# Performance work log

Hardware: AMD Instinct MI355X
Metric: run time of the kernel (lower is better)

## Reference

```python
import jax, jax.numpy as jnp
import numpy as np

BATCH, T, HID = 4, 2048, 1024
H = P = 1024  # input_dim and ssm_size (expand_ratio=1.0)
EPS = 1e-5
DISCRETIZATION = "IM"  # 'IM' or 'IMEX'


def setup_inputs() -> dict:
    key = jax.random.key(0)
    ks = jax.random.split(key, 10)
    std_b = 1.0 / np.sqrt(H)
    std_c = 1.0 / np.sqrt(P)
    u = lambda k, s, lo, hi: jax.random.uniform(k, s, jnp.float32, lo, hi)
    return {
        "hidden_states": jax.random.normal(ks[0], (BATCH, T, HID), jnp.float32),
        "Wi": jax.random.normal(ks[1], (H, HID), jnp.float32) / np.sqrt(HID),
        "Wg": jax.random.normal(ks[2], (H, HID), jnp.float32) / np.sqrt(HID),
        "Wo": jax.random.normal(ks[3], (HID, H), jnp.float32) / np.sqrt(H),
        "A_diag": u(ks[4], (P,), 0.0, 1.0),
        "B_param": u(ks[5], (P, H, 2), -std_b, std_b),
        "C_param": u(ks[6], (H, P, 2), -std_c, std_c),
        "D": jax.random.normal(ks[7], (H,), jnp.float32),
        "dt": u(ks[8], (P,), 0.0, 1.0),
        "norm_weight": jnp.ones((H,), jnp.float32),
    }


def _linoss(x, B_param, C_param, A_diag, dt_p, D):
    """LinOSS oscillatory SSM recurrence with complex B/C and diagonal A.
    x: (B,T,H) real input. State z,y in C^P (re/im stacked on last axis)."""
    A = jax.nn.relu(A_diag)       # (P,) nonneg frequencies
    dt = jax.nn.sigmoid(dt_p)     # (P,) timesteps in (0,1)
    # Bu_{re,im}[b,t,p] = sum_h x[b,t,h] * B_{re,im}[p,h]
    Bu = jnp.einsum('bth,phc->btpc', x, B_param)  # (B,T,P,2)
    if DISCRETIZATION == "IM":
        S = 1.0 / (1.0 + dt * dt * A)
        m11, m12, m21, m22 = S, -dt * A * S, dt * S, S
        f1, f2 = dt * S, dt * dt * S
    else:  # IMEX
        one = jnp.ones_like(dt)
        m11, m12, m21, m22 = one, -dt * A, dt, 1.0 - dt * dt * A
        f1, f2 = dt, dt * dt
    c = lambda v: v[None, :, None]  # broadcast (P,) -> (B,P,2)

    def step(carry, bu):
        z, y = carry  # each (B,P,2)
        z1 = c(m11) * z + c(m12) * y + c(f1) * bu
        y1 = c(m21) * z + c(m22) * y + c(f2) * bu
        return (z1, y1), y1

    z0 = jnp.zeros((x.shape[0], A.shape[0], 2), x.dtype)
    _, ys = jax.lax.scan(step, (z0, z0), jnp.swapaxes(Bu, 0, 1))
    ys = jnp.swapaxes(ys, 0, 1)  # (B,T,P,2)
    # o = Re(C @ y) + D * x
    o = (jnp.einsum('btp,hp->bth', ys[..., 0], C_param[..., 0])
         - jnp.einsum('btp,hp->bth', ys[..., 1], C_param[..., 1]))
    return o + x * D


def reference(hidden_states, Wi, Wg, Wo, A_diag, B_param, C_param, D, dt, norm_weight):
    x = hidden_states @ Wi.T                        # i_proj
    o = _linoss(x, B_param, C_param, A_diag, dt, D)  # fused_recurrent_linoss
    g = hidden_states @ Wg.T                        # g_proj
    # FusedRMSNormGated: rmsnorm(o) * weight * swish(g)
    o = o * jax.lax.rsqrt(jnp.mean(o * o, axis=-1, keepdims=True) + EPS) * norm_weight
    o = o * (g * jax.nn.sigmoid(g))
    return o @ Wo.T                                  # o_proj
```

## Files before the change

kernel.cpp:

```cpp
#include <hip/hip_runtime.h>
#include <hip/hip_bf16.h>
#include <math.h>

#define BB 4
#define TT 2048
#define HH 1024
#define PP 1024
#define MT 8192
#define C2 2048
#define NC 64
#define LCH 32

typedef __attribute__((ext_vector_type(8))) short  bf16x8;
typedef __attribute__((ext_vector_type(4))) float  f32x4;

__device__ __forceinline__ ushort f2bf(float f) {
    union { float f; unsigned u; } v; v.f = f;
    unsigned r = v.u + 0x7fffu + ((v.u >> 16) & 1u);
    return (ushort)(r >> 16);
}
__device__ __forceinline__ float bf2f(ushort h) {
    union { unsigned u; float f; } v; v.u = ((unsigned)h) << 16;
    return v.f;
}

__device__ __forceinline__ void gload16(const ushort* g, ushort* l) {
    __builtin_amdgcn_global_load_lds((const __attribute__((address_space(1))) void*)g,
                                     (__attribute__((address_space(3))) void*)l,
                                     16, 0, 0);
}
__device__ __forceinline__ void barrier_raw() { __builtin_amdgcn_s_barrier(); }
__device__ __forceinline__ void lgk0() { asm volatile("s_waitcnt lgkmcnt(0)" ::: "memory"); }
__device__ __forceinline__ void vm4()  { asm volatile("s_waitcnt vmcnt(4)"   ::: "memory"); }
__device__ __forceinline__ void vm6()  { asm volatile("s_waitcnt vmcnt(6)"   ::: "memory"); }
__device__ __forceinline__ void vm0()  { asm volatile("s_waitcnt vmcnt(0)"   ::: "memory"); }

__global__ void convert_all(const float* __restrict__ hs, const float* __restrict__ Wi,
                            const float* __restrict__ Wg, const float* __restrict__ Wo,
                            ushort* __restrict__ hsb, ushort* __restrict__ Wigb,
                            ushort* __restrict__ Wob) {
    int i = blockIdx.x * 256 + threadIdx.x;
    const int HS4 = MT * HH / 4;
    const int W4  = HH * HH / 4;
    const float4* s;
    ushort4* d;
    if (i < HS4)               { s = (const float4*)hs + i;               d = (ushort4*)hsb  + i; }
    else if (i < HS4 + 2 * W4) { int j = i - HS4;
                                 s = (const float4*)(j < W4 ? Wi : Wg) + (j < W4 ? j : j - W4);
                                 d = (ushort4*)Wigb + j; }
    else                       { int j = i - HS4 - 2 * W4;
                                 s = (const float4*)Wo + j;               d = (ushort4*)Wob + j; }
    float4 v = *s;
    ushort4 o;
    o.x = f2bf(v.x); o.y = f2bf(v.y); o.z = f2bf(v.z); o.w = f2bf(v.w);
    *d = o;
}

__global__ void repack_B_bf(const float* __restrict__ src, ushort* __restrict__ dst) {
    int idx = blockIdx.x * 256 + threadIdx.x;
    int p = idx >> 10;
    int h = idx & 1023;
    float2 v = ((const float2*)src)[idx];
    dst[(size_t)p * HH + h]        = f2bf(v.x);
    dst[(size_t)(p + PP) * HH + h] = f2bf(v.y);
}

__global__ void repack_C_bf(const float* __restrict__ src, ushort* __restrict__ dst) {
    int idx = blockIdx.x * 256 + threadIdx.x;
    int h = idx >> 10;
    int p = idx & 1023;
    float2 v = ((const float2*)src)[idx];
    dst[(size_t)h * C2 + p]      = f2bf(v.x);
    dst[(size_t)h * C2 + PP + p] = f2bf(-v.y);
}

template<int BM, int STORE_BF16>
__global__ __launch_bounds__(512, 2) void gemm8p(
    const ushort* __restrict__ A, int lda,
    const ushort* __restrict__ B, int ldb,
    void* __restrict__ Cp, int ldc, int K, int nbx)
{
    constexpr int BN  = 256;
    constexpr int MR  = BM / 32;
    constexpr int MRH = MR / 2;
    constexpr int TA  = BM * 128;
    constexpr int TB  = BN * 128;
    __shared__ __align__(16) char smem[2 * TA + 2 * TB];

    const int bid = blockIdx.x;
    const int cpx = gridDim.x >> 3;
    const int wg  = (bid & 7) * cpx + (bid >> 3);
    const int by  = wg / nbx;
    const int bx  = wg - by * nbx;
    const int bm  = by * BM;
    const int bn  = bx * BN;

    const int tid  = threadIdx.x;
    const int wave = tid >> 6;
    const int lane = tid & 63;
    const int wr   = wave >> 2;
    const int wc   = wave & 3;
    const int lr   = lane & 15;
    const int kg   = lane >> 4;

    const int e  = (wave << 10) + ((lane << 4) ^ (((lane >> 3) & 7) << 4));
    const int r0 = e >> 7;
    const int c0 = (e & 127) >> 1;

    auto stA = [&](int bi, int u, int kt) {
        gload16(A + (size_t)(bm + u * 64 + r0) * lda + kt * 64 + c0,
                (ushort*)(smem + bi * TA + u * 8192 + (wave << 10)));
    };
    auto stB = [&](int bi, int u, int kt) {
        gload16(B + (size_t)(bn + u * 64 + r0) * ldb + kt * 64 + c0,
                (ushort*)(smem + 2 * TA + bi * TB + u * 8192 + (wave << 10)));
    };

    bf16x8 Af[MRH][2], Bf[4][2];
    auto ldsA = [&](int bi, int qm) {
#pragma unroll
        for (int f = 0; f < MRH; ++f)
#pragma unroll
            for (int kk = 0; kk < 2; ++kk) {
                int row = wr * (BM / 2) + qm * (BM / 4) + f * 16 + lr;
                int o = row * 128 + kk * 64 + kg * 16;
                o ^= (row & 7) << 4;
                Af[f][kk] = *(const bf16x8*)(smem + bi * TA + o);
            }
    };
    auto ldsB = [&](int bi) {
#pragma unroll
        for (int n = 0; n < 4; ++n)
#pragma unroll
            for (int kk = 0; kk < 2; ++kk) {
                int row = wc * 64 + n * 16 + lr;
                int o = row * 128 + kk * 64 + kg * 16;
                o ^= (row & 7) << 4;
                Bf[n][kk] = *(const bf16x8*)(smem + 2 * TA + bi * TB + o);
            }
    };

    f32x4 acc[MR][4];
#pragma unroll
    for (int m = 0; m < MR; ++m)
#pragma unroll
        for (int n = 0; n < 4; ++n)
#pragma unroll
            for (int i = 0; i < 4; ++i) acc[m][n][i] = 0.f;

    auto mfma16 = [&](int qm, int qn) {
        __builtin_amdgcn_s_setprio(1);
#pragma unroll
        for (int f = 0; f < MRH; ++f)
#pragma unroll
            for (int n2 = 0; n2 < 2; ++n2)
#pragma unroll
                for (int kk = 0; kk < 2; ++kk)
                    acc[qm * MRH + f][qn * 2 + n2] =
                        __builtin_amdgcn_mfma_f32_16x16x32_bf16(
                            Af[f][kk], Bf[qn * 2 + n2][kk],
                            acc[qm * MRH + f][qn * 2 + n2], 0, 0, 0);
        __builtin_amdgcn_s_setprio(0);
    };

    if constexpr (BM == 256) {
        stA(0, 0, 0); stA(0, 1, 0); stA(0, 2, 0); stA(0, 3, 0);
        stB(0, 0, 0); stB(0, 1, 0); stB(0, 2, 0); stB(0, 3, 0);
        stB(1, 0, 1); stB(1, 1, 1); stB(1, 2, 1); stB(1, 3, 1);
        stA(1, 0, 1); stA(1, 2, 1);
    } else {
        stA(0, 0, 0); stA(0, 1, 0);
        stB(0, 0, 0); stB(0, 1, 0); stB(0, 2, 0); stB(0, 3, 0);
        stA(1, 0, 1); stA(1, 1, 1);
        stB(1, 0, 1); stB(1, 1, 1); stB(1, 2, 1); stB(1, 3, 1);
    }
    vm6();
    barrier_raw();

    const int nIter = K >> 7;
    for (int J = 0; J < nIter; ++J) {
        const bool pf  = (J + 1 < nIter);
        const int  kt1 = 2 * J + 1, kt2 = 2 * J + 2, kt3 = 2 * J + 3;
        ldsA(0, 0); ldsB(0);
        if constexpr (BM == 256) { stA(1, 1, kt1); stA(1, 3, kt1); }
        barrier_raw(); lgk0(); mfma16(0, 0); barrier_raw();
        if (pf) { stB(0, 0, kt2); stB(0, 1, kt2); }
        barrier_raw(); lgk0(); mfma16(0, 1); barrier_raw();
        ldsA(0, 1);
        if (pf) { stB(0, 2, kt2); stB(0, 3, kt2); }
        barrier_raw(); lgk0(); mfma16(1, 0); barrier_raw();
        if (pf) {
            if constexpr (BM == 256) { stA(0, 0, kt2); stA(0, 2, kt2); }
            else                     { stA(0, 0, kt2); stA(0, 1, kt2); }
        }
        barrier_raw(); lgk0(); mfma16(1, 1);
        if (pf) vm6(); else vm0();
        barrier_raw();
        ldsA(1, 0); ldsB(1);
        if constexpr (BM == 256) { if (pf) { stA(0, 1, kt2); stA(0, 3, kt2); } }
        barrier_raw(); lgk0(); mfma16(0, 0); barrier_raw();
        if (pf) { stB(1, 0, kt3); stB(1, 1, kt3); }
        barrier_raw(); lgk0(); mfma16(0, 1); barrier_raw();
        ldsA(1, 1);
        if (pf) { stB(1, 2, kt3); stB(1, 3, kt3); }
        barrier_raw(); lgk0(); mfma16(1, 0); barrier_raw();
        if (pf) {
            if constexpr (BM == 256) { stA(1, 0, kt3); stA(1, 2, kt3); }
            else                     { stA(1, 0, kt3); stA(1, 1, kt3); }
        }
        barrier_raw(); lgk0(); mfma16(1, 1);
        if (pf) vm6(); else vm0();
        barrier_raw();
    }

#pragma unroll
    for (int mf = 0; mf < MR; ++mf) {
#pragma unroll
        for (int n = 0; n < 4; ++n) {
            int col = bn + wc * 64 + n * 16 + lr;
#pragma unroll
            for (int i = 0; i < 4; ++i) {
                int row = bm + wr * (BM / 2) + mf * 16 + kg * 4 + i;
                float v = acc[mf][n][i];
                if (STORE_BF16)
                    ((ushort*)Cp)[(size_t)row * ldc + col] = f2bf(v);
                else
                    ((float*)Cp)[(size_t)row * ldc + col]  = v;
            }
        }
    }
}

template<int STORE_BF16>
__global__ __launch_bounds__(512, 2) void gemm4p(
    const ushort* __restrict__ A, int lda,
    const ushort* __restrict__ B, int ldb,
    void* __restrict__ Cp, int ldc, int K, int nbx)
{
    constexpr int BM = 128, BN = 256;
    constexpr int TA = BM * 128;
    constexpr int TB = BN * 128;
    __shared__ __align__(16) char smem[2 * TA + 2 * TB];

    const int bid = blockIdx.x;
    const int cpx = gridDim.x >> 3;
    const int wg  = (bid & 7) * cpx + (bid >> 3);
    const int by  = wg / nbx;
    const int bx  = wg - by * nbx;
    const int bm  = by * BM;
    const int bn  = bx * BN;

    const int tid  = threadIdx.x;
    const int wave = tid >> 6;
    const int lane = tid & 63;
    const int wr   = wave >> 2;
    const int wc   = wave & 3;
    const int lr   = lane & 15;
    const int kg   = lane >> 4;

    const int e  = (wave << 10) + ((lane << 4) ^ (((lane >> 3) & 7) << 4));
    const int r0 = e >> 7;
    const int c0 = (e & 127) >> 1;

    auto stA = [&](int bi, int u, int kt) {
        gload16(A + (size_t)(bm + u * 64 + r0) * lda + kt * 64 + c0,
                (ushort*)(smem + bi * TA + u * 8192 + (wave << 10)));
    };
    auto stB = [&](int bi, int u, int kt) {
        gload16(B + (size_t)(bn + u * 64 + r0) * ldb + kt * 64 + c0,
                (ushort*)(smem + 2 * TA + bi * TB + u * 8192 + (wave << 10)));
    };

    bf16x8 Af[2][2], Bf[4][2];
    auto ldsA = [&](int bi, int qm) {
#pragma unroll
        for (int f = 0; f < 2; ++f)
#pragma unroll
            for (int kk = 0; kk < 2; ++kk) {
                int row = wr * 64 + qm * 32 + f * 16 + lr;
                int o = row * 128 + kk * 64 + kg * 16;
                o ^= (row & 7) << 4;
                Af[f][kk] = *(const bf16x8*)(smem + bi * TA + o);
            }
    };
    auto ldsB = [&](int bi) {
#pragma unroll
        for (int n = 0; n < 4; ++n)
#pragma unroll
            for (int kk = 0; kk < 2; ++kk) {
                int row = wc * 64 + n * 16 + lr;
                int o = row * 128 + kk * 64 + kg * 16;
                o ^= (row & 7) << 4;
                Bf[n][kk] = *(const bf16x8*)(smem + 2 * TA + bi * TB + o);
            }
    };

    f32x4 acc[4][4];
#pragma unroll
    for (int m = 0; m < 4; ++m)
#pragma unroll
        for (int n = 0; n < 4; ++n)
#pragma unroll
            for (int i = 0; i < 4; ++i) acc[m][n][i] = 0.f;

    auto cl = [&](int qm) {
        __builtin_amdgcn_s_setprio(1);
#pragma unroll
        for (int f = 0; f < 2; ++f)
#pragma unroll
            for (int n = 0; n < 4; ++n)
#pragma unroll
                for (int kk = 0; kk < 2; ++kk)
                    acc[qm * 2 + f][n] =
                        __builtin_amdgcn_mfma_f32_16x16x32_bf16(
                            Af[f][kk], Bf[n][kk], acc[qm * 2 + f][n], 0, 0, 0);
        __builtin_amdgcn_s_setprio(0);
    };

    stB(0, 0, 0); stB(0, 1, 0); stB(0, 2, 0); stB(0, 3, 0);
    stA(0, 0, 0); stA(0, 1, 0);
    stB(1, 0, 1); stB(1, 1, 1); stB(1, 2, 1); stB(1, 3, 1);
    vm4();
    barrier_raw();

    const int nIter = K >> 7;
    for (int J = 0; J < nIter; ++J) {
        const bool pf  = (J + 1 < nIter);
        const int  kt1 = 2 * J + 1, kt2 = 2 * J + 2, kt3 = 2 * J + 3;
        ldsA(0, 0); ldsB(0);
        stA(1, 0, kt1); stA(1, 1, kt1);
        barrier_raw();
        cl(0);
        lgk0();
        barrier_raw();
        ldsA(0, 1);
        if (pf) { stB(0, 0, kt2); stB(0, 1, kt2); stB(0, 2, kt2); stB(0, 3, kt2); }
        barrier_raw();
        cl(1);
        lgk0();
        if (pf) vm4(); else vm0();
        barrier_raw();
        ldsA(1, 0); ldsB(1);
        if (pf) { stA(0, 0, kt2); stA(0, 1, kt2); }
        barrier_raw();
        cl(0);
        lgk0();
        barrier_raw();
        ldsA(1, 1);
        if (pf) { stB(1, 0, kt3); stB(1, 1, kt3); stB(1, 2, kt3); stB(1, 3, kt3); }
        barrier_raw();
        cl(1);
        lgk0();
        if (pf) vm4();
        barrier_raw();
    }

#pragma unroll
    for (int mf = 0; mf < 4; ++mf) {
#pragma unroll
        for (int n = 0; n < 4; ++n) {
            int col = bn + wc * 64 + n * 16 + lr;
#pragma unroll
            for (int i = 0; i < 4; ++i) {
                int row = bm + wr * 64 + mf * 16 + kg * 4 + i;
                float v = acc[mf][n][i];
                if (STORE_BF16)
                    ((ushort*)Cp)[(size_t)row * ldc + col] = f2bf(v);
                else
                    ((float*)Cp)[(size_t)row * ldc + col]  = v;
            }
        }
    }
}

__device__ __forceinline__ void linoss_coeffs(const float* A_diag, const float* dt_p,
                                              int p, float& m11, float& m12,
                                              float& m21, float& m22,
                                              float& f1, float& f2) {
    float A  = fmaxf(A_diag[p], 0.f);
    float dt = 1.f / (1.f + expf(-dt_p[p]));
    float S  = 1.f / (1.f + dt * dt * A);
    m11 = S;        m12 = -dt * A * S;
    m21 = dt * S;   m22 = S;
    f1  = dt * S;   f2  = dt * dt * S;
}

__global__ void scan_passA(const ushort* __restrict__ Bu,
                           const float* __restrict__ A_diag,
                           const float* __restrict__ dt_p,
                           float2* __restrict__ sEnd) {
    int c = blockIdx.x * 256 + threadIdx.x;
    int b = blockIdx.y;
    int j = blockIdx.z;
    float m11, m12, m21, m22, f1, f2;
    linoss_coeffs(A_diag, dt_p, c & 1023, m11, m12, m21, m22, f1, f2);
    const ushort* bu = Bu + ((size_t)(b * TT + j * LCH)) * C2 + c;
    float z = 0.f, y = 0.f;
#pragma unroll 8
    for (int i = 0; i < LCH; ++i) {
        float u  = bf2f(bu[(size_t)i * C2]);
        float z1 = m11 * z + m12 * y + f1 * u;
        float y1 = m21 * z + m22 * y + f2 * u;
        z = z1; y = y1;
    }
    sEnd[((size_t)j * BB + b) * C2 + c] = make_float2(z, y);
}

__global__ void scan_combine(const float* __restrict__ A_diag,
                             const float* __restrict__ dt_p,
                             const float2* __restrict__ sEnd,
                             float2* __restrict__ sInit) {
    int idx = blockIdx.x * 256 + threadIdx.x;
    int c = idx & (C2 - 1);
    int b = idx >> 11;
    float m11, m12, m21, m22, f1, f2;
    linoss_coeffs(A_diag, dt_p, c & 1023, m11, m12, m21, m22, f1, f2);
    float e11 = m11, e12 = m12, e21 = m21, e22 = m22;
#pragma unroll
    for (int s = 0; s < 5; ++s) {
        float n11 = e11 * e11 + e12 * e21;
        float n12 = e11 * e12 + e12 * e22;
        float n21 = e21 * e11 + e22 * e21;
        float n22 = e21 * e12 + e22 * e22;
        e11 = n11; e12 = n12; e21 = n21; e22 = n22;
    }
    float z = 0.f, y = 0.f;
    for (int j = 0; j < NC; ++j) {
        size_t off = ((size_t)j * BB + b) * C2 + c;
        sInit[off] = make_float2(z, y);
        float2 le = sEnd[off];
        float z1 = e11 * z + e12 * y + le.x;
        float y1 = e21 * z + e22 * y + le.y;
        z = z1; y = y1;
    }
}

__global__ void scan_passB(const ushort* __restrict__ Bu,
                           const float* __restrict__ A_diag,
                           const float* __restrict__ dt_p,
                           const float2* __restrict__ sInit,
                           ushort* __restrict__ YSb) {
    int c = blockIdx.x * 256 + threadIdx.x;
    int b = blockIdx.y;
    int j = blockIdx.z;
    float m11, m12, m21, m22, f1, f2;
    linoss_coeffs(A_diag, dt_p, c & 1023, m11, m12, m21, m22, f1, f2);
    float2 s0 = sInit[((size_t)j * BB + b) * C2 + c];
    float z = s0.x, y = s0.y;
    const ushort* bu = Bu  + ((size_t)(b * TT + j * LCH)) * C2 + c;
    ushort*       ys = YSb + ((size_t)(b * TT + j * LCH)) * C2 + c;
#pragma unroll 8
    for (int i = 0; i < LCH; ++i) {
        float u  = bf2f(bu[(size_t)i * C2]);
        float z1 = m11 * z + m12 * y + f1 * u;
        float y1 = m21 * z + m22 * y + f2 * u;
        z = z1; y = y1;
        ys[(size_t)i * C2] = f2bf(y);
    }
}

__global__ void rmsgate_kernel(const ushort* __restrict__ O,
                               const ushort* __restrict__ XGb,
                               const float* __restrict__ Dv,
                               const float* __restrict__ nw,
                               ushort* __restrict__ V) {
    int m = blockIdx.x;
    int t = threadIdx.x;
    ushort4 o4 = ((const ushort4*)(O + (size_t)m * HH))[t];
    ushort4 x4 = ((const ushort4*)(XGb + (size_t)m * C2))[t];
    float4  d4 = ((const float4*)Dv)[t];
    float of[4];
    of[0] = bf2f(o4.x) + d4.x * bf2f(x4.x);
    of[1] = bf2f(o4.y) + d4.y * bf2f(x4.y);
    of[2] = bf2f(o4.z) + d4.z * bf2f(x4.z);
    of[3] = bf2f(o4.w) + d4.w * bf2f(x4.w);
    float ss = of[0]*of[0] + of[1]*of[1] + of[2]*of[2] + of[3]*of[3];
#pragma unroll
    for (int o = 32; o > 0; o >>= 1) ss += __shfl_down(ss, o);
    __shared__ float wsum[4];
    if ((t & 63) == 0) wsum[t >> 6] = ss;
    __syncthreads();
    float tot = wsum[0] + wsum[1] + wsum[2] + wsum[3];
    float r = rsqrtf(tot * (1.f / (float)HH) + 1e-5f);

    ushort4 g4 = ((const ushort4*)(XGb + (size_t)m * C2 + HH))[t];
    float4  w4 = ((const float4*)nw)[t];
    float g[4] = {bf2f(g4.x), bf2f(g4.y), bf2f(g4.z), bf2f(g4.w)};
    float w[4] = {w4.x, w4.y, w4.z, w4.w};
    ushort4 vout;
    ushort* vo = &vout.x;
#pragma unroll
    for (int i = 0; i < 4; ++i) {
        float sw = g[i] / (1.f + expf(-g[i]));
        vo[i] = f2bf(of[i] * r * w[i] * sw);
    }
    ((ushort4*)(V + (size_t)m * HH))[t] = vout;
}

extern "C" void kernel_launch(void* const* d_in, const int* in_sizes, int n_in,
                              void* d_out, int out_size, void* d_ws, size_t ws_size,
                              hipStream_t stream) {
    const float* hs      = (const float*)d_in[0];
    const float* Wi      = (const float*)d_in[1];
    const float* Wg      = (const float*)d_in[2];
    const float* Wo      = (const float*)d_in[3];
    const float* A_diag  = (const float*)d_in[4];
    const float* B_param = (const float*)d_in[5];
    const float* C_param = (const float*)d_in[6];
    const float* Dv      = (const float*)d_in[7];
    const float* dtp     = (const float*)d_in[8];
    const float* nw      = (const float*)d_in[9];
    float* out = (float*)d_out;

    char* ws = (char*)d_ws;
    ushort* hsb  = (ushort*)ws;                                   ws += (size_t)MT * HH * 2;
    ushort* Wigb = (ushort*)ws;                                   ws += (size_t)C2 * HH * 2;
    ushort* Wob  = (ushort*)ws;                                   ws += (size_t)HH * HH * 2;
    ushort* Bpkb = (ushort*)ws;                                   ws += (size_t)C2 * HH * 2;
    ushort* Cpkb = (ushort*)ws;                                   ws += (size_t)HH * C2 * 2;
    ushort* XGb  = (ushort*)ws;                                   ws += (size_t)MT * C2 * 2;
    ushort* Bu   = (ushort*)ws;                                   ws += (size_t)MT * C2 * 2;
    ushort* YSb  = (ushort*)ws;                                   ws += (size_t)MT * C2 * 2;
    ushort* O    = (ushort*)ws;                                   ws += (size_t)MT * HH * 2;
    ushort* Vb   = (ushort*)ws;                                   ws += (size_t)MT * HH * 2;
    float2* sEnd  = (float2*)ws;                                  ws += (size_t)NC * BB * C2 * 8;
    float2* sInit = (float2*)ws;

    dim3 blk(256);

    convert_all<<<dim3((MT * HH / 4 + 3 * HH * HH / 4) / 256), blk, 0, stream>>>(
        hs, Wi, Wg, Wo, hsb, Wigb, Wob);
    repack_B_bf<<<dim3((PP * HH) / 256), blk, 0, stream>>>(B_param, Bpkb);
    repack_C_bf<<<dim3((HH * PP) / 256), blk, 0, stream>>>(C_param, Cpkb);

    gemm8p<256, 1><<<dim3(256), dim3(512), 0, stream>>>(
        hsb, HH, Wigb, HH, XGb, C2, HH, 8);

    gemm8p<256, 1><<<dim3(256), dim3(512), 0, stream>>>(
        XGb, C2, Bpkb, HH, Bu, C2, HH, 8);

    scan_passA<<<dim3(C2 / 256, BB, NC), blk, 0, stream>>>(Bu, A_diag, dtp, sEnd);
    scan_combine<<<dim3((BB * C2) / 256), blk, 0, stream>>>(A_diag, dtp, sEnd, sInit);
    scan_passB<<<dim3(C2 / 256, BB, NC), blk, 0, stream>>>(Bu, A_diag, dtp, sInit, YSb);

    gemm4p<1><<<dim3(256), dim3(512), 0, stream>>>(
        YSb, C2, Cpkb, C2, O, HH, C2, 4);

    rmsgate_kernel<<<dim3(MT), blk, 0, stream>>>(O, XGb, Dv, nw, Vb);

    gemm4p<0><<<dim3(256), dim3(512), 0, stream>>>(
        Vb, HH, Wob, HH, out, HH, HH, 4);
}
```

Baseline: 191.3 us.

## Merge prep kernels and restage gemm8p B-tile LDS loads and prefetches

Merges the three conversion/repack launches into one prep_all kernel, removing two launches. In gemm8p, B-fragment LDS reads are split into two halves that are loaded just before the MFMA quarter that uses them, and the global B prefetches are grouped into one later phase. Partial lgkmcnt(8) waits are inserted before barriers in both GEMMs so they do not wait on every outstanding LDS read at once. The reordering changes how latency is hidden and relies on the hand-picked wait counts matching the actual number of outstanding memory operations.

Result: no change. 188.1 us (-1.6%).

```diff
diff --git a/kernel.cpp b/kernel.cpp
--- a/kernel.cpp
+++ b/kernel.cpp
@@ -31,47 +31,52 @@
 }
 __device__ __forceinline__ void barrier_raw() { __builtin_amdgcn_s_barrier(); }
 __device__ __forceinline__ void lgk0() { asm volatile("s_waitcnt lgkmcnt(0)" ::: "memory"); }
+__device__ __forceinline__ void lgk8() { asm volatile("s_waitcnt lgkmcnt(8)" ::: "memory"); }
 __device__ __forceinline__ void vm4()  { asm volatile("s_waitcnt vmcnt(4)"   ::: "memory"); }
 __device__ __forceinline__ void vm6()  { asm volatile("s_waitcnt vmcnt(6)"   ::: "memory"); }
 __device__ __forceinline__ void vm0()  { asm volatile("s_waitcnt vmcnt(0)"   ::: "memory"); }
 
-__global__ void convert_all(const float* __restrict__ hs, const float* __restrict__ Wi,
-                            const float* __restrict__ Wg, const float* __restrict__ Wo,
-                            ushort* __restrict__ hsb, ushort* __restrict__ Wigb,
-                            ushort* __restrict__ Wob) {
+#define HS4   (MT * HH / 4)
+#define W4    (HH * HH / 4)
+#define PREP_CONV  (HS4 + 3 * W4)
+#define PREP_B     (PREP_CONV + PP * HH)
+#define PREP_TOT   (PREP_B + HH * PP)
+
+__global__ void prep_all(const float* __restrict__ hs, const float* __restrict__ Wi,
+                         const float* __restrict__ Wg, const float* __restrict__ Wo,
+                         const float* __restrict__ B_param, const float* __restrict__ C_param,
+                         ushort* __restrict__ hsb, ushort* __restrict__ Wigb,
+                         ushort* __restrict__ Wob, ushort* __restrict__ Bpkb,
+                         ushort* __restrict__ Cpkb) {
     int i = blockIdx.x * 256 + threadIdx.x;
-    const int HS4 = MT * HH / 4;
-    const int W4  = HH * HH / 4;
-    const float4* s;
-    ushort4* d;
-    if (i < HS4)               { s = (const float4*)hs + i;               d = (ushort4*)hsb  + i; }
-    else if (i < HS4 + 2 * W4) { int j = i - HS4;
-                                 s = (const float4*)(j < W4 ? Wi : Wg) + (j < W4 ? j : j - W4);
-                                 d = (ushort4*)Wigb + j; }
-    else                       { int j = i - HS4 - 2 * W4;
-                                 s = (const float4*)Wo + j;               d = (ushort4*)Wob + j; }
-    float4 v = *s;
-    ushort4 o;
-    o.x = f2bf(v.x); o.y = f2bf(v.y); o.z = f2bf(v.z); o.w = f2bf(v.w);
-    *d = o;
-}
-
-__global__ void repack_B_bf(const float* __restrict__ src, ushort* __restrict__ dst) {
-    int idx = blockIdx.x * 256 + threadIdx.x;
-    int p = idx >> 10;
-    int h = idx & 1023;
-    float2 v = ((const float2*)src)[idx];
-    dst[(size_t)p * HH + h]        = f2bf(v.x);
-    dst[(size_t)(p + PP) * HH + h] = f2bf(v.y);
-}
-
-__global__ void repack_C_bf(const float* __restrict__ src, ushort* __restrict__ dst) {
-    int idx = blockIdx.x * 256 + threadIdx.x;
-    int h = idx >> 10;
-    int p = idx & 1023;
-    float2 v = ((const float2*)src)[idx];
-    dst[(size_t)h * C2 + p]      = f2bf(v.x);
-    dst[(size_t)h * C2 + PP + p] = f2bf(-v.y);
+    if (i < PREP_CONV) {
+        const float4* s;
+        ushort4* d;
+        if (i < HS4)              { s = (const float4*)hs + i;  d = (ushort4*)hsb + i; }
+        else if (i < HS4 + 2*W4)  { int j = i - HS4;
+                                    s = (const float4*)(j < W4 ? Wi : Wg) + (j < W4 ? j : j - W4);
+                                    d = (ushort4*)Wigb + j; }
+        else                      { int j = i - HS4 - 2*W4;
+                                    s = (const float4*)Wo + j; d = (ushort4*)Wob + j; }
+        float4 v = *s;
+        ushort4 o;
+        o.x = f2bf(v.x); o.y = f2bf(v.y); o.z = f2bf(v.z); o.w = f2bf(v.w);
+        *d = o;
+    } else if (i < PREP_B) {
+        int idx = i - PREP_CONV;
+        int p = idx >> 10;
+        int h = idx & 1023;
+        float2 v = ((const float2*)B_param)[idx];
+        Bpkb[(size_t)p * HH + h]        = f2bf(v.x);
+        Bpkb[(size_t)(p + PP) * HH + h] = f2bf(v.y);
+    } else {
+        int idx = i - PREP_B;
+        int h = idx >> 10;
+        int p = idx & 1023;
+        float2 v = ((const float2*)C_param)[idx];
+        Cpkb[(size_t)h * C2 + p]      = f2bf(v.x);
+        Cpkb[(size_t)h * C2 + PP + p] = f2bf(-v.y);
+    }
 }
 
 template<int BM, int STORE_BF16>
@@ -128,15 +133,15 @@
                 Af[f][kk] = *(const bf16x8*)(smem + bi * TA + o);
             }
     };
-    auto ldsB = [&](int bi) {
-#pragma unroll
-        for (int n = 0; n < 4; ++n)
+    auto ldsBh = [&](int bi, int h) {
+#pragma unroll
+        for (int n = 0; n < 2; ++n)
 #pragma unroll
             for (int kk = 0; kk < 2; ++kk) {
-                int row = wc * 64 + n * 16 + lr;
+                int row = wc * 64 + (h * 2 + n) * 16 + lr;
                 int o = row * 128 + kk * 64 + kg * 16;
                 o ^= (row & 7) << 4;
-                Bf[n][kk] = *(const bf16x8*)(smem + 2 * TA + bi * TB + o);
+                Bf[h * 2 + n][kk] = *(const bf16x8*)(smem + 2 * TA + bi * TB + o);
             }
     };
 
@@ -163,17 +168,10 @@
         __builtin_amdgcn_s_setprio(0);
     };
 
-    if constexpr (BM == 256) {
-        stA(0, 0, 0); stA(0, 1, 0); stA(0, 2, 0); stA(0, 3, 0);
-        stB(0, 0, 0); stB(0, 1, 0); stB(0, 2, 0); stB(0, 3, 0);
-        stB(1, 0, 1); stB(1, 1, 1); stB(1, 2, 1); stB(1, 3, 1);
-        stA(1, 0, 1); stA(1, 2, 1);
-    } else {
-        stA(0, 0, 0); stA(0, 1, 0);
-        stB(0, 0, 0); stB(0, 1, 0); stB(0, 2, 0); stB(0, 3, 0);
-        stA(1, 0, 1); stA(1, 1, 1);
-        stB(1, 0, 1); stB(1, 1, 1); stB(1, 2, 1); stB(1, 3, 1);
-    }
+    stA(0, 0, 0); stA(0, 1, 0); stA(0, 2, 0); stA(0, 3, 0);
+    stB(0, 0, 0); stB(0, 1, 0); stB(0, 2, 0); stB(0, 3, 0);
+    stB(1, 0, 1); stB(1, 1, 1); stB(1, 2, 1); stB(1, 3, 1);
+    stA(1, 0, 1); stA(1, 2, 1);
     vm6();
     barrier_raw();
 
@@ -181,33 +179,29 @@
     for (int J = 0; J < nIter; ++J) {
         const bool pf  = (J + 1 < nIter);
         const int  kt1 = 2 * J + 1, kt2 = 2 * J + 2, kt3 = 2 * J + 3;
-        ldsA(0, 0); ldsB(0);
-        if constexpr (BM == 256) { stA(1, 1, kt1); stA(1, 3, kt1); }
+        ldsA(0, 0); ldsBh(0, 0);
+        stA(1, 1, kt1); stA(1, 3, kt1);
+        lgk8();
         barrier_raw(); lgk0(); mfma16(0, 0); barrier_raw();
-        if (pf) { stB(0, 0, kt2); stB(0, 1, kt2); }
+        ldsBh(0, 1);
         barrier_raw(); lgk0(); mfma16(0, 1); barrier_raw();
         ldsA(0, 1);
-        if (pf) { stB(0, 2, kt2); stB(0, 3, kt2); }
+        if (pf) { stB(0, 0, kt2); stB(0, 1, kt2); stB(0, 2, kt2); stB(0, 3, kt2); }
         barrier_raw(); lgk0(); mfma16(1, 0); barrier_raw();
-        if (pf) {
-            if constexpr (BM == 256) { stA(0, 0, kt2); stA(0, 2, kt2); }
-            else                     { stA(0, 0, kt2); stA(0, 1, kt2); }
-        }
+        if (pf) { stA(0, 0, kt2); stA(0, 2, kt2); }
         barrier_raw(); lgk0(); mfma16(1, 1);
         if (pf) vm6(); else vm0();
         barrier_raw();
-        ldsA(1, 0); ldsB(1);
-        if constexpr (BM == 256) { if (pf) { stA(0, 1, kt2); stA(0, 3, kt2); } }
+        ldsA(1, 0); ldsBh(1, 0);
+        if (pf) { stA(0, 1, kt2); stA(0, 3, kt2); }
+        lgk8();
         barrier_raw(); lgk0(); mfma16(0, 0); barrier_raw();
-        if (pf) { stB(1, 0, kt3); stB(1, 1, kt3); }
+        ldsBh(1, 1);
         barrier_raw(); lgk0(); mfma16(0, 1); barrier_raw();
         ldsA(1, 1);
-        if (pf) { stB(1, 2, kt3); stB(1, 3, kt3); }
+        if (pf) { stB(1, 0, kt3); stB(1, 1, kt3); stB(1, 2, kt3); stB(1, 3, kt3); }
         barrier_raw(); lgk0(); mfma16(1, 0); barrier_raw();
-        if (pf) {
-            if constexpr (BM == 256) { stA(1, 0, kt3); stA(1, 2, kt3); }
-            else                     { stA(1, 0, kt3); stA(1, 1, kt3); }
-        }
+        if (pf) { stA(1, 0, kt3); stA(1, 2, kt3); }
         barrier_raw(); lgk0(); mfma16(1, 1);
         if (pf) vm6(); else vm0();
         barrier_raw();
@@ -329,6 +323,7 @@
         const int  kt1 = 2 * J + 1, kt2 = 2 * J + 2, kt3 = 2 * J + 3;
         ldsA(0, 0); ldsB(0);
         stA(1, 0, kt1); stA(1, 1, kt1);
+        lgk8();
         barrier_raw();
         cl(0);
         lgk0();
@@ -342,6 +337,7 @@
         barrier_raw();
         ldsA(1, 0); ldsB(1);
         if (pf) { stA(0, 0, kt2); stA(0, 1, kt2); }
+        lgk8();
         barrier_raw();
         cl(0);
         lgk0();
@@ -528,10 +524,8 @@
 
     dim3 blk(256);
 
-    convert_all<<<dim3((MT * HH / 4 + 3 * HH * HH / 4) / 256), blk, 0, stream>>>(
-        hs, Wi, Wg, Wo, hsb, Wigb, Wob);
-    repack_B_bf<<<dim3((PP * HH) / 256), blk, 0, stream>>>(B_param, Bpkb);
-    repack_C_bf<<<dim3((HH * PP) / 256), blk, 0, stream>>>(C_param, Cpkb);
+    prep_all<<<dim3(PREP_TOT / 256), blk, 0, stream>>>(
+        hs, Wi, Wg, Wo, B_param, C_param, hsb, Wigb, Wob, Bpkb, Cpkb);
 
     gemm8p<256, 1><<<dim3(256), dim3(512), 0, stream>>>(
         hsb, HH, Wigb, HH, XGb, C2, HH, 8);
```
